# Kernel tuning notes

Hardware: AMD Instinct MI355X
Metric: run time of the kernel (lower is better)

The kernel has to match this reference:

```python
import jax, jax.numpy as jnp
import numpy as np

B, S, D = 2, 2048, 1024
H = 16
HD = D // H  # 64
ROPE_BASE = 10000.0


def rotate_half(x):
    x1, x2 = jnp.split(x, 2, axis=-1)
    return jnp.concatenate((-x2, x1), axis=-1)


def rope_cos_sin(seq_len, dim, dtype):
    inv_freq = 1.0 / (ROPE_BASE ** (jnp.arange(0, dim, 2, dtype=jnp.float32) / dim))
    t = jnp.arange(seq_len, dtype=jnp.float32)
    freqs = jnp.einsum('i,j->ij', t, inv_freq)          # [S, dim/2]
    emb = jnp.concatenate((freqs, freqs), axis=-1)      # [S, dim]
    return jnp.cos(emb).astype(dtype), jnp.sin(emb).astype(dtype)


def setup_inputs() -> dict:
    key = jax.random.key(0)
    ks = jax.random.split(key, 5)
    std = 0.02
    return {
        'x': jax.random.normal(ks[0], (B, S, D), dtype=jnp.float32),
        'wq': jax.random.normal(ks[1], (D, D), dtype=jnp.float32) * std,
        'wk': jax.random.normal(ks[2], (D, D), dtype=jnp.float32) * std,
        'wv': jax.random.normal(ks[3], (D, D), dtype=jnp.float32) * std,
        'wo': jax.random.normal(ks[4], (D, D), dtype=jnp.float32) * std,
    }


def reference(x, wq, wk, wv, wo):
    b, s, d = x.shape
    # Q/K/V projections (nn.Linear: x @ W.T)
    q = jnp.einsum('bsd,ed->bse', x, wq).reshape(b, s, H, HD).transpose(0, 2, 1, 3)
    k = jnp.einsum('bsd,ed->bse', x, wk).reshape(b, s, H, HD).transpose(0, 2, 1, 3)
    v = jnp.einsum('bsd,ed->bse', x, wv).reshape(b, s, H, HD).transpose(0, 2, 1, 3)
    # RoPE
    cos, sin = rope_cos_sin(s, HD, x.dtype)  # [s, HD]
    cos = cos[None, None]  # [1,1,s,HD]
    sin = sin[None, None]
    q = q * cos + rotate_half(q) * sin
    k = k * cos + rotate_half(k) * sin
    # Causal SDPA
    scale = HD ** -0.5
    scores = jnp.einsum('bhqd,bhkd->bhqk', q, k) * scale
    causal = jnp.tril(jnp.ones((s, s), dtype=bool))
    scores = jnp.where(causal[None, None], scores, jnp.finfo(scores.dtype).min)
    attn = jax.nn.softmax(scores, axis=-1)
    out = jnp.einsum('bhqk,bhkd->bhqd', attn, v)
    out = out.transpose(0, 2, 1, 3).reshape(b, s, d)
    return jnp.einsum('bsd,ed->bse', out, wo)
```

## Files before the change

### kernel.cpp

```cpp
#include <hip/hip_runtime.h>
#include <hip/hip_bf16.h>
#include <cstdint>
#include <cstddef>

#define BDIM 2
#define SDIM 2048
#define DDIM 1024
#define HN   16
#define HDIM 64

using bf16 = __bf16;
typedef __attribute__((ext_vector_type(8))) __bf16 bf16x8;
typedef __attribute__((ext_vector_type(4))) __bf16 bf16x4;
typedef __attribute__((ext_vector_type(8))) unsigned short ushort8;
typedef __attribute__((ext_vector_type(4))) float  f32x4;

#define MFMA16(a, b, c) __builtin_amdgcn_mfma_f32_16x16x32_bf16((a), (b), (c), 0, 0, 0)

#define ASYNC16(g, l)                                                          \
  __builtin_amdgcn_global_load_lds(                                            \
      (const __attribute__((address_space(1))) void*)(g),                      \
      (__attribute__((address_space(3))) void*)(l), 16, 0, 0)

#define QSCALE 0.1803368801111204f

__global__ __launch_bounds__(256) void cvt_bf16(const float* __restrict__ src,
                                                bf16* __restrict__ dst, int n4) {
  int i = blockIdx.x * 256 + threadIdx.x;
  if (i < n4) {
    float4 v = ((const float4*)src)[i];
    bf16x4 o = {(__bf16)v.x, (__bf16)v.y, (__bf16)v.z, (__bf16)v.w};
    *(bf16x4*)(dst + (size_t)i * 4) = o;
  }
}

struct Ptr4 { const float* p[4]; };
__global__ __launch_bounds__(256) void cvt_w(Ptr4 srcs, bf16* __restrict__ dst) {
  const int seg = blockIdx.y;
  const float* src = srcs.p[seg];
  int i = blockIdx.x * 256 + threadIdx.x;
  float4 v = ((const float4*)src)[i];
  bf16x4 o = {(__bf16)v.x, (__bf16)v.y, (__bf16)v.z, (__bf16)v.w};
  *(bf16x4*)(dst + (size_t)seg * (DDIM * DDIM) + (size_t)i * 4) = o;
}

__global__ __launch_bounds__(256) void rope_table(float* __restrict__ cosT,
                                                  float* __restrict__ sinT) {
  int i = blockIdx.x * 256 + threadIdx.x;
  int s = i >> 5, j = i & 31;
  float inv = powf(10000.f, -(float)j * (1.f / 32.f));
  float a = (float)s * inv;
  float sn, c;
  sincosf(a, &sn, &c);
  cosT[s * 64 + j]      = c;
  cosT[s * 64 + j + 32] = c;
  sinT[s * 64 + j]      = sn;
  sinT[s * 64 + j + 32] = sn;
}

__global__ __launch_bounds__(256) void rope_apply(bf16* __restrict__ q,
                                                  bf16* __restrict__ k,
                                                  const float* __restrict__ cosT,
                                                  const float* __restrict__ sinT) {
  int i = blockIdx.x * 256 + threadIdx.x;
  int j = i & 31;
  int s = (i >> 5) & (SDIM - 1);
  int bh = i >> 16;
  size_t base = ((size_t)bh * SDIM + s) * HDIM;
  float c = cosT[s * 64 + j], sn = sinT[s * 64 + j];
  float a = (float)q[base + j], b2 = (float)q[base + j + 32];
  q[base + j]      = (__bf16)((a * c - b2 * sn) * QSCALE);
  q[base + j + 32] = (__bf16)((b2 * c + a * sn) * QSCALE);
  a = (float)k[base + j]; b2 = (float)k[base + j + 32];
  k[base + j]      = (__bf16)(a * c - b2 * sn);
  k[base + j + 32] = (__bf16)(b2 * c + a * sn);
}

__global__ __launch_bounds__(256) void transpose_v(const unsigned short* __restrict__ v,
                                                   unsigned short* __restrict__ vt) {
  const int bh = blockIdx.y;
  const int s_base = blockIdx.x * 32 + (threadIdx.x >> 6) * 8;
  const int d = threadIdx.x & 63;
  const unsigned short* src = v + ((size_t)bh * SDIM + s_base) * HDIM + d;
  ushort8 o;
#pragma unroll
  for (int j = 0; j < 8; ++j) o[j] = src[(size_t)j * HDIM];
  *(ushort8*)(vt + ((size_t)bh * HDIM + d) * SDIM + s_base) = o;
}

template <int MODE>
__global__ __launch_bounds__(256) void gemm_bt(const bf16* __restrict__ A,
                                               const bf16* __restrict__ B0,
                                               void* __restrict__ C0) {
  constexpr int K = 1024;
  __shared__ __align__(16) bf16 As[128 * 64];
  __shared__ __align__(16) bf16 Bs[128 * 64];
  const int tid = threadIdx.x;
  const int l = tid & 63, w = tid >> 6;
  const int wr = w >> 1, wc = w & 1;
  const int lr = l & 15, lg = l >> 4;
  const int bm = blockIdx.y * 128;
  const int bn = blockIdx.x * 128;
  const bf16* Bw = B0 + (size_t)blockIdx.z * (1024 * 1024);

  f32x4 acc[4][4] = {};

  for (int k0 = 0; k0 < K; k0 += 64) {
    __syncthreads();
#pragma unroll
    for (int i = 0; i < 4; ++i) {
      int idx = i * 2048 + tid * 8;
      int row = idx >> 6, col = idx & 63;
      ASYNC16(A + (size_t)(bm + row) * K + (k0 + col), As + idx);
      ASYNC16(Bw + (size_t)(bn + row) * K + (k0 + col), Bs + idx);
    }
    __syncthreads();
#pragma unroll
    for (int c = 0; c < 2; ++c) {
      bf16x8 af[4], bfr[4];
#pragma unroll
      for (int m = 0; m < 4; ++m)
        af[m] = *(const bf16x8*)(As + (wr * 64 + m * 16 + lr) * 64 + c * 32 + lg * 8);
#pragma unroll
      for (int n = 0; n < 4; ++n)
        bfr[n] = *(const bf16x8*)(Bs + (wc * 64 + n * 16 + lr) * 64 + c * 32 + lg * 8);
      __builtin_amdgcn_s_setprio(1);
#pragma unroll
      for (int m = 0; m < 4; ++m)
#pragma unroll
        for (int n = 0; n < 4; ++n)
          acc[m][n] = MFMA16(af[m], bfr[n], acc[m][n]);
      __builtin_amdgcn_s_setprio(0);
    }
  }

#pragma unroll
  for (int m = 0; m < 4; ++m) {
#pragma unroll
    for (int n = 0; n < 4; ++n) {
#pragma unroll
      for (int r = 0; r < 4; ++r) {
        int row = bm + wr * 64 + m * 16 + lg * 4 + r;
        int col = bn + wc * 64 + n * 16 + lr;
        float v = acc[m][n][r];
        if constexpr (MODE == 0) {
          bf16* C = (bf16*)C0 + (size_t)blockIdx.z * ((size_t)BDIM * SDIM * DDIM);
          size_t off = (((size_t)(row >> 11) * HN + (col >> 6)) * SDIM + (row & (SDIM - 1))) * HDIM + (col & 63);
          C[off] = (__bf16)v;
        } else {
          ((float*)C0)[(size_t)row * DDIM + col] = v;
        }
      }
    }
  }
}

__global__ __launch_bounds__(256) void attn_fwd(const bf16* __restrict__ qg,
                                                const bf16* __restrict__ kg,
                                                const bf16* __restrict__ vtg,
                                                bf16* __restrict__ og) {
  __shared__ __align__(16) bf16 Ks[2][8 * 512];
  __shared__ __align__(16) bf16 Vs[2][8 * 512];
  __shared__ __align__(16) bf16 Pl[4][16 * 72];

  const int tid = threadIdx.x;
  const int l = tid & 63, w = tid >> 6;
  const int lr = l & 15, lg = l >> 4;
  const int lin = blockIdx.x + (blockIdx.y << 4);
  const int bh = lin & 31;
  const int qp = lin >> 5;
  const size_t hb = (size_t)bh * SDIM * HDIM;
  const bf16* Q  = qg + hb;
  const bf16* Kp = kg + hb;
  const bf16* Vp = vtg + hb;
  const int b = bh >> 4, h = bh & 15;
  bf16* Pw = &Pl[w][0];

  const int mm0 = 2 * w, mm1 = 2 * w + 1;
  const int f0 = mm0 & 3, c0 = mm0 >> 2;
  const int f1 = mm1 & 3, c1 = mm1 >> 2;
  bf16* const kd0_0 = Ks[0] + mm0 * 512 + l * 8;
  bf16* const kd1_0 = Ks[0] + mm1 * 512 + l * 8;
  bf16* const vd0_0 = Vs[0] + mm0 * 512 + l * 8;
  bf16* const vd1_0 = Vs[0] + mm1 * 512 + l * 8;

  for (int phase = 0; phase < 2; ++phase) {
    const int qt = phase ? (31 - qp) : qp;
    const int q0 = qt * 64;

    bf16x8 qf[2];
#pragma unroll
    for (int c = 0; c < 2; ++c)
      qf[c] = *(const bf16x8*)(Q + (size_t)(q0 + w * 16 + lr) * HDIM + c * 32 + lg * 8);

    f32x4 o[4] = {};
    float m = -3e38f, lsum = 0.f;

    const bf16* kN0 = Kp + (size_t)(f0 * 16 + lr) * HDIM + c0 * 32 + lg * 8;
    const bf16* kN1 = Kp + (size_t)(f1 * 16 + lr) * HDIM + c1 * 32 + lg * 8;
    const bf16* vN0 = Vp + (size_t)(f0 * 16 + lr) * SDIM + c0 * 32 + lg * 8;
    const bf16* vN1 = Vp + (size_t)(f1 * 16 + lr) * SDIM + c1 * 32 + lg * 8;

    ASYNC16(kN0, kd0_0); kN0 += 64 * HDIM;
    ASYNC16(kN1, kd1_0); kN1 += 64 * HDIM;
    ASYNC16(vN0, vd0_0); vN0 += 64;
    ASYNC16(vN1, vd1_0); vN1 += 64;
    __syncthreads();

    for (int t = 0; t <= qt; ++t) {
      const int cur = t & 1;
      if (t < qt) {
        bf16* kd = Ks[cur ^ 1];
        bf16* vd = Vs[cur ^ 1];
        ASYNC16(kN0, kd + mm0 * 512 + l * 8); kN0 += 64 * HDIM;
        ASYNC16(kN1, kd + mm1 * 512 + l * 8); kN1 += 64 * HDIM;
        ASYNC16(vN0, vd + mm0 * 512 + l * 8); vN0 += 64;
        ASYNC16(vN1, vd + mm1 * 512 + l * 8); vN1 += 64;
      }

      const bool diag = (t == qt);
      const int fLim = diag ? w : 3;

      f32x4 sc[4] = {};
      __builtin_amdgcn_s_setprio(1);
#pragma unroll
      for (int c = 0; c < 2; ++c)
#pragma unroll
        for (int f = 0; f < 4; ++f)
          if (f <= fLim) {
            bf16x8 kfr = *(const bf16x8*)(Ks[cur] + (c * 4 + f) * 512 + l * 8);
            sc[f] = MFMA16(kfr, qf[c], sc[f]);
          }
      __builtin_amdgcn_s_setprio(0);

      if (diag) {
#pragma unroll
        for (int f = 0; f < 4; ++f)
#pragma unroll
          for (int r = 0; r < 4; ++r) {
            if (f > w)
              sc[f][r] = -3e38f;
            else if (f == w)
              sc[f][r] = (lg * 4 + r <= lr) ? sc[f][r] : -3e38f;
          }
      }

      float mx = -3e38f;
#pragma unroll
      for (int f = 0; f < 4; ++f)
#pragma unroll
        for (int r = 0; r < 4; ++r) mx = fmaxf(mx, sc[f][r]);
      mx = fmaxf(mx, __shfl_xor(mx, 16));
      mx = fmaxf(mx, __shfl_xor(mx, 32));

      if (!__all(mx - m <= 8.f)) {
        float mnew = fmaxf(m, mx);
        float corr = exp2f(m - mnew);
        m = mnew;
        lsum *= corr;
        float cb[4];
#pragma unroll
        for (int r = 0; r < 4; ++r) cb[r] = __shfl(corr, lg * 4 + r);
#pragma unroll
        for (int n = 0; n < 4; ++n)
#pragma unroll
          for (int r = 0; r < 4; ++r) o[n][r] *= cb[r];
      }

      float rs = 0.f;
#pragma unroll
      for (int f = 0; f < 4; ++f) {
        float p0 = exp2f(sc[f][0] - m);
        float p1 = exp2f(sc[f][1] - m);
        float p2 = exp2f(sc[f][2] - m);
        float p3 = exp2f(sc[f][3] - m);
        rs += (p0 + p1) + (p2 + p3);
        bf16x4 pv = {(__bf16)p0, (__bf16)p1, (__bf16)p2, (__bf16)p3};
        *(bf16x4*)(Pw + lr * 72 + f * 16 + lg * 4) = pv;
      }
      rs += __shfl_xor(rs, 16);
      rs += __shfl_xor(rs, 32);
      lsum += rs;

      const int cLim = diag ? (w >> 1) : 1;
      __builtin_amdgcn_s_setprio(1);
#pragma unroll
      for (int c = 0; c < 2; ++c)
        if (c <= cLim) {
          bf16x8 pf = *(const bf16x8*)(Pw + lr * 72 + c * 32 + lg * 8);
#pragma unroll
          for (int n = 0; n < 4; ++n) {
            bf16x8 vfr = *(const bf16x8*)(Vs[cur] + (c * 4 + n) * 512 + l * 8);
            o[n] = MFMA16(pf, vfr, o[n]);
          }
        }
      __builtin_amdgcn_s_setprio(0);

      __syncthreads();
    }

    float lb[4];
#pragma unroll
    for (int r = 0; r < 4; ++r) lb[r] = __shfl(lsum, lg * 4 + r);
#pragma unroll
    for (int r = 0; r < 4; ++r) {
      float rl = 1.f / lb[r];
      int qr = q0 + 16 * w + lg * 4 + r;
#pragma unroll
      for (int n = 0; n < 4; ++n)
        og[((size_t)(b * SDIM + qr)) * DDIM + h * HDIM + n * 16 + lr] =
            (__bf16)(o[n][r] * rl);
    }
  }
}

extern "C" void kernel_launch(void* const* d_in, const int* in_sizes, int n_in,
                              void* d_out, int out_size, void* d_ws, size_t ws_size,
                              hipStream_t stream) {
  const float* x  = (const float*)d_in[0];
  const float* wq = (const float*)d_in[1];
  const float* wk = (const float*)d_in[2];
  const float* wv = (const float*)d_in[3];
  const float* wo = (const float*)d_in[4];

  char* ws = (char*)d_ws;
  const size_t MB = 1024 * 1024;
  bf16* xb   = (bf16*)(ws + 0);
  bf16* wqb  = (bf16*)(ws + 8 * MB);
  bf16* wob  = (bf16*)(ws + 14 * MB);
  bf16* qb   = (bf16*)(ws + 16 * MB);
  bf16* kb   = (bf16*)(ws + 24 * MB);
  bf16* vb   = (bf16*)(ws + 32 * MB);
  bf16* ob   = (bf16*)(ws + 40 * MB);
  float* cosT = (float*)(ws + 48 * MB);
  float* sinT = (float*)(ws + 49 * MB);
  bf16* vtb  = xb;

  const int NX = BDIM * SDIM * DDIM;
  const int NW = DDIM * DDIM;

  cvt_bf16<<<NX / 4 / 256, 256, 0, stream>>>(x, xb, NX / 4);
  Ptr4 wsrc{{wq, wk, wv, wo}};
  cvt_w<<<dim3(NW / 4 / 256, 4), 256, 0, stream>>>(wsrc, wqb);
  rope_table<<<(SDIM * 32) / 256, 256, 0, stream>>>(cosT, sinT);
  gemm_bt<0><<<dim3(8, 32, 3), 256, 0, stream>>>(xb, wqb, (void*)qb);
  rope_apply<<<(32 * SDIM * 32) / 256, 256, 0, stream>>>(qb, kb, cosT, sinT);
  transpose_v<<<dim3(SDIM / 32, 32), 256, 0, stream>>>((const unsigned short*)vb,
                                                       (unsigned short*)vtb);
  attn_fwd<<<dim3(16, 32), 256, 0, stream>>>(qb, kb, vtb, ob);
  gemm_bt<1><<<dim3(8, 32, 1), 256, 0, stream>>>(ob, wob, d_out);
}
```

Before: 148.9 us.

## Fuse RoPE and V transpose into QKV GEMM epilogue

Applies RoPE (with the Q scale folded into a precomputed cos/sin table) directly in the QKV projection epilogue, pairing accumulator columns j and j+32 that the same wave holds. V is written already transposed from the GEMM epilogue, which removes the rope_apply and transpose_v kernels and their global memory round trips. The attention kernel also defers the cross-lane max shuffles until a rescale is actually needed. The epilogue stores become scattered, and the deferred max relies on a per-lane bound check staying conservative.

New measurement: 153.7 us. +3.2%, slower.

```diff
diff --git a/kernel.cpp b/kernel.cpp
--- a/kernel.cpp
+++ b/kernel.cpp
@@ -12,7 +12,6 @@
 using bf16 = __bf16;
 typedef __attribute__((ext_vector_type(8))) __bf16 bf16x8;
 typedef __attribute__((ext_vector_type(4))) __bf16 bf16x4;
-typedef __attribute__((ext_vector_type(8))) unsigned short ushort8;
 typedef __attribute__((ext_vector_type(4))) float  f32x4;
 
 #define MFMA16(a, b, c) __builtin_amdgcn_mfma_f32_16x16x32_bf16((a), (b), (c), 0, 0, 0)
@@ -44,54 +43,24 @@
   *(bf16x4*)(dst + (size_t)seg * (DDIM * DDIM) + (size_t)i * 4) = o;
 }
 
-__global__ __launch_bounds__(256) void rope_table(float* __restrict__ cosT,
-                                                  float* __restrict__ sinT) {
+__global__ __launch_bounds__(256) void rope_table(float2* __restrict__ cq,
+                                                  float2* __restrict__ ck) {
   int i = blockIdx.x * 256 + threadIdx.x;
   int s = i >> 5, j = i & 31;
   float inv = powf(10000.f, -(float)j * (1.f / 32.f));
   float a = (float)s * inv;
   float sn, c;
   sincosf(a, &sn, &c);
-  cosT[s * 64 + j]      = c;
-  cosT[s * 64 + j + 32] = c;
-  sinT[s * 64 + j]      = sn;
-  sinT[s * 64 + j + 32] = sn;
-}
-
-__global__ __launch_bounds__(256) void rope_apply(bf16* __restrict__ q,
-                                                  bf16* __restrict__ k,
-                                                  const float* __restrict__ cosT,
-                                                  const float* __restrict__ sinT) {
-  int i = blockIdx.x * 256 + threadIdx.x;
-  int j = i & 31;
-  int s = (i >> 5) & (SDIM - 1);
-  int bh = i >> 16;
-  size_t base = ((size_t)bh * SDIM + s) * HDIM;
-  float c = cosT[s * 64 + j], sn = sinT[s * 64 + j];
-  float a = (float)q[base + j], b2 = (float)q[base + j + 32];
-  q[base + j]      = (__bf16)((a * c - b2 * sn) * QSCALE);
-  q[base + j + 32] = (__bf16)((b2 * c + a * sn) * QSCALE);
-  a = (float)k[base + j]; b2 = (float)k[base + j + 32];
-  k[base + j]      = (__bf16)(a * c - b2 * sn);
-  k[base + j + 32] = (__bf16)(b2 * c + a * sn);
-}
-
-__global__ __launch_bounds__(256) void transpose_v(const unsigned short* __restrict__ v,
-                                                   unsigned short* __restrict__ vt) {
-  const int bh = blockIdx.y;
-  const int s_base = blockIdx.x * 32 + (threadIdx.x >> 6) * 8;
-  const int d = threadIdx.x & 63;
-  const unsigned short* src = v + ((size_t)bh * SDIM + s_base) * HDIM + d;
-  ushort8 o;
-#pragma unroll
-  for (int j = 0; j < 8; ++j) o[j] = src[(size_t)j * HDIM];
-  *(ushort8*)(vt + ((size_t)bh * HDIM + d) * SDIM + s_base) = o;
+  ck[i] = make_float2(c, sn);
+  cq[i] = make_float2(c * QSCALE, sn * QSCALE);
 }
 
 template <int MODE>
 __global__ __launch_bounds__(256) void gemm_bt(const bf16* __restrict__ A,
                                                const bf16* __restrict__ B0,
-                                               void* __restrict__ C0) {
+                                               void* __restrict__ C0,
+                                               const float2* __restrict__ cq,
+                                               const float2* __restrict__ ck) {
   constexpr int K = 1024;
   __shared__ __align__(16) bf16 As[128 * 64];
   __shared__ __align__(16) bf16 Bs[128 * 64];
@@ -134,24 +103,53 @@
     }
   }
 
-#pragma unroll
-  for (int m = 0; m < 4; ++m) {
-#pragma unroll
-    for (int n = 0; n < 4; ++n) {
-#pragma unroll
-      for (int r = 0; r < 4; ++r) {
-        int row = bm + wr * 64 + m * 16 + lg * 4 + r;
-        int col = bn + wc * 64 + n * 16 + lr;
-        float v = acc[m][n][r];
-        if constexpr (MODE == 0) {
-          bf16* C = (bf16*)C0 + (size_t)blockIdx.z * ((size_t)BDIM * SDIM * DDIM);
-          size_t off = (((size_t)(row >> 11) * HN + (col >> 6)) * SDIM + (row & (SDIM - 1))) * HDIM + (col & 63);
-          C[off] = (__bf16)v;
-        } else {
-          ((float*)C0)[(size_t)row * DDIM + col] = v;
+  if constexpr (MODE == 0) {
+    const int z = blockIdx.z;
+    bf16* C = (bf16*)C0 + (size_t)z * ((size_t)BDIM * SDIM * DDIM);
+    if (z == 2) {
+#pragma unroll
+      for (int m = 0; m < 4; ++m)
+#pragma unroll
+        for (int n = 0; n < 4; ++n) {
+          int row0 = bm + wr * 64 + m * 16 + lg * 4;
+          int col  = bn + wc * 64 + n * 16 + lr;
+          int bb = row0 >> 11, s0 = row0 & (SDIM - 1);
+          int h = col >> 6, hd = col & 63;
+          bf16x4 pv = {(__bf16)acc[m][n][0], (__bf16)acc[m][n][1],
+                       (__bf16)acc[m][n][2], (__bf16)acc[m][n][3]};
+          *(bf16x4*)(C + ((size_t)(bb * HN + h) * HDIM + hd) * SDIM + s0) = pv;
         }
-      }
-    }
+    } else {
+      const float2* tab = z ? ck : cq;
+#pragma unroll
+      for (int m = 0; m < 4; ++m)
+#pragma unroll
+        for (int n = 0; n < 2; ++n) {
+          int j = n * 16 + lr;
+          int h = (bn >> 6) + wc;
+#pragma unroll
+          for (int r = 0; r < 4; ++r) {
+            int row = bm + wr * 64 + m * 16 + lg * 4 + r;
+            int s = row & (SDIM - 1), bb = row >> 11;
+            float2 cs = tab[s * 32 + j];
+            float a = acc[m][n][r], b2 = acc[m][n + 2][r];
+            size_t base = ((size_t)(bb * HN + h) * SDIM + s) * HDIM;
+            C[base + j]      = (__bf16)(a * cs.x - b2 * cs.y);
+            C[base + j + 32] = (__bf16)(b2 * cs.x + a * cs.y);
+          }
+        }
+    }
+  } else {
+#pragma unroll
+    for (int m = 0; m < 4; ++m)
+#pragma unroll
+      for (int n = 0; n < 4; ++n)
+#pragma unroll
+        for (int r = 0; r < 4; ++r) {
+          int row = bm + wr * 64 + m * 16 + lg * 4 + r;
+          int col = bn + wc * 64 + n * 16 + lr;
+          ((float*)C0)[(size_t)row * DDIM + col] = acc[m][n][r];
+        }
   }
 }
 
@@ -245,15 +243,15 @@
           }
       }
 
-      float mx = -3e38f;
+      float mxl = -3e38f;
 #pragma unroll
       for (int f = 0; f < 4; ++f)
 #pragma unroll
-        for (int r = 0; r < 4; ++r) mx = fmaxf(mx, sc[f][r]);
-      mx = fmaxf(mx, __shfl_xor(mx, 16));
-      mx = fmaxf(mx, __shfl_xor(mx, 32));
-
-      if (!__all(mx - m <= 8.f)) {
+        for (int r = 0; r < 4; ++r) mxl = fmaxf(mxl, sc[f][r]);
+
+      if (!__all(mxl - m <= 8.f)) {
+        float mx = fmaxf(mxl, __shfl_xor(mxl, 16));
+        mx = fmaxf(mx, __shfl_xor(mx, 32));
         float mnew = fmaxf(m, mx);
         float corr = exp2f(m - mnew);
         m = mnew;
@@ -330,11 +328,10 @@
   bf16* wob  = (bf16*)(ws + 14 * MB);
   bf16* qb   = (bf16*)(ws + 16 * MB);
   bf16* kb   = (bf16*)(ws + 24 * MB);
-  bf16* vb   = (bf16*)(ws + 32 * MB);
+  bf16* vtb  = (bf16*)(ws + 32 * MB);
   bf16* ob   = (bf16*)(ws + 40 * MB);
-  float* cosT = (float*)(ws + 48 * MB);
-  float* sinT = (float*)(ws + 49 * MB);
-  bf16* vtb  = xb;
+  float2* cqT = (float2*)(ws + 48 * MB);
+  float2* ckT = (float2*)(ws + 48 * MB + 512 * 1024);
 
   const int NX = BDIM * SDIM * DDIM;
   const int NW = DDIM * DDIM;
@@ -342,11 +339,8 @@
   cvt_bf16<<<NX / 4 / 256, 256, 0, stream>>>(x, xb, NX / 4);
   Ptr4 wsrc{{wq, wk, wv, wo}};
   cvt_w<<<dim3(NW / 4 / 256, 4), 256, 0, stream>>>(wsrc, wqb);
-  rope_table<<<(SDIM * 32) / 256, 256, 0, stream>>>(cosT, sinT);
-  gemm_bt<0><<<dim3(8, 32, 3), 256, 0, stream>>>(xb, wqb, (void*)qb);
-  rope_apply<<<(32 * SDIM * 32) / 256, 256, 0, stream>>>(qb, kb, cosT, sinT);
-  transpose_v<<<dim3(SDIM / 32, 32), 256, 0, stream>>>((const unsigned short*)vb,
-                                                       (unsigned short*)vtb);
+  rope_table<<<(SDIM * 32) / 256, 256, 0, stream>>>(cqT, ckT);
+  gemm_bt<0><<<dim3(8, 32, 3), 256, 0, stream>>>(xb, wqb, (void*)qb, cqT, ckT);
   attn_fwd<<<dim3(16, 32), 256, 0, stream>>>(qb, kb, vtb, ob);
-  gemm_bt<1><<<dim3(8, 32, 1), 256, 0, stream>>>(ob, wob, d_out);
-}
+  gemm_bt<1><<<dim3(8, 32, 1), 256, 0, stream>>>(ob, wob, d_out, nullptr, nullptr);
+}
```

## Launch one block per query tile with longest-first order and swizzled P buffer

Applied to the files above, without the earlier changes.

Each attention block used to process two paired query tiles (qp and 31-qp) to balance the causal work. Now every block handles a single query tile, so the grid doubles to 1024 blocks, ordered so the heaviest (largest qt) tiles go out first. The P scratch buffer drops its 72-element padding in favour of an XOR swizzle to avoid LDS bank conflicts. The max reduction across lanes is also moved inside the rescale branch, so the common path skips two shuffles. The trade-off is losing the explicit pairing balance and relying on the hardware scheduler to even out tile lengths.

Measured after the change: 145.8 us. 2.1% less time.

```diff
diff --git a/kernel.cpp b/kernel.cpp
--- a/kernel.cpp
+++ b/kernel.cpp
@@ -161,156 +161,149 @@
                                                 bf16* __restrict__ og) {
   __shared__ __align__(16) bf16 Ks[2][8 * 512];
   __shared__ __align__(16) bf16 Vs[2][8 * 512];
-  __shared__ __align__(16) bf16 Pl[4][16 * 72];
+  __shared__ __align__(16) bf16 Pl[4][16 * 64];
 
   const int tid = threadIdx.x;
   const int l = tid & 63, w = tid >> 6;
   const int lr = l & 15, lg = l >> 4;
-  const int lin = blockIdx.x + (blockIdx.y << 4);
-  const int bh = lin & 31;
-  const int qp = lin >> 5;
+  const int bh = blockIdx.x;
+  const int qt = 31 - blockIdx.y;
+  const int q0 = qt * 64;
   const size_t hb = (size_t)bh * SDIM * HDIM;
   const bf16* Q  = qg + hb;
   const bf16* Kp = kg + hb;
   const bf16* Vp = vtg + hb;
   const int b = bh >> 4, h = bh & 15;
   bf16* Pw = &Pl[w][0];
+  const int swz = lr & 7;
 
   const int mm0 = 2 * w, mm1 = 2 * w + 1;
   const int f0 = mm0 & 3, c0 = mm0 >> 2;
   const int f1 = mm1 & 3, c1 = mm1 >> 2;
-  bf16* const kd0_0 = Ks[0] + mm0 * 512 + l * 8;
-  bf16* const kd1_0 = Ks[0] + mm1 * 512 + l * 8;
-  bf16* const vd0_0 = Vs[0] + mm0 * 512 + l * 8;
-  bf16* const vd1_0 = Vs[0] + mm1 * 512 + l * 8;
-
-  for (int phase = 0; phase < 2; ++phase) {
-    const int qt = phase ? (31 - qp) : qp;
-    const int q0 = qt * 64;
-
-    bf16x8 qf[2];
+
+  bf16x8 qf[2];
+#pragma unroll
+  for (int c = 0; c < 2; ++c)
+    qf[c] = *(const bf16x8*)(Q + (size_t)(q0 + w * 16 + lr) * HDIM + c * 32 + lg * 8);
+
+  f32x4 o[4] = {};
+  float m = -3e38f, lsum = 0.f;
+
+  const bf16* kN0 = Kp + (size_t)(f0 * 16 + lr) * HDIM + c0 * 32 + lg * 8;
+  const bf16* kN1 = Kp + (size_t)(f1 * 16 + lr) * HDIM + c1 * 32 + lg * 8;
+  const bf16* vN0 = Vp + (size_t)(f0 * 16 + lr) * SDIM + c0 * 32 + lg * 8;
+  const bf16* vN1 = Vp + (size_t)(f1 * 16 + lr) * SDIM + c1 * 32 + lg * 8;
+
+  ASYNC16(kN0, Ks[0] + mm0 * 512 + l * 8); kN0 += 64 * HDIM;
+  ASYNC16(kN1, Ks[0] + mm1 * 512 + l * 8); kN1 += 64 * HDIM;
+  ASYNC16(vN0, Vs[0] + mm0 * 512 + l * 8); vN0 += 64;
+  ASYNC16(vN1, Vs[0] + mm1 * 512 + l * 8); vN1 += 64;
+  __syncthreads();
+
+  for (int t = 0; t <= qt; ++t) {
+    const int cur = t & 1;
+    if (t < qt) {
+      bf16* kd = Ks[cur ^ 1];
+      bf16* vd = Vs[cur ^ 1];
+      ASYNC16(kN0, kd + mm0 * 512 + l * 8); kN0 += 64 * HDIM;
+      ASYNC16(kN1, kd + mm1 * 512 + l * 8); kN1 += 64 * HDIM;
+      ASYNC16(vN0, vd + mm0 * 512 + l * 8); vN0 += 64;
+      ASYNC16(vN1, vd + mm1 * 512 + l * 8); vN1 += 64;
+    }
+
+    const bool diag = (t == qt);
+    const int fLim = diag ? w : 3;
+
+    f32x4 sc[4] = {};
+    __builtin_amdgcn_s_setprio(1);
 #pragma unroll
     for (int c = 0; c < 2; ++c)
-      qf[c] = *(const bf16x8*)(Q + (size_t)(q0 + w * 16 + lr) * HDIM + c * 32 + lg * 8);
-
-    f32x4 o[4] = {};
-    float m = -3e38f, lsum = 0.f;
-
-    const bf16* kN0 = Kp + (size_t)(f0 * 16 + lr) * HDIM + c0 * 32 + lg * 8;
-    const bf16* kN1 = Kp + (size_t)(f1 * 16 + lr) * HDIM + c1 * 32 + lg * 8;
-    const bf16* vN0 = Vp + (size_t)(f0 * 16 + lr) * SDIM + c0 * 32 + lg * 8;
-    const bf16* vN1 = Vp + (size_t)(f1 * 16 + lr) * SDIM + c1 * 32 + lg * 8;
-
-    ASYNC16(kN0, kd0_0); kN0 += 64 * HDIM;
-    ASYNC16(kN1, kd1_0); kN1 += 64 * HDIM;
-    ASYNC16(vN0, vd0_0); vN0 += 64;
-    ASYNC16(vN1, vd1_0); vN1 += 64;
+#pragma unroll
+      for (int f = 0; f < 4; ++f)
+        if (f <= fLim) {
+          bf16x8 kfr = *(const bf16x8*)(Ks[cur] + (c * 4 + f) * 512 + l * 8);
+          sc[f] = MFMA16(kfr, qf[c], sc[f]);
+        }
+    __builtin_amdgcn_s_setprio(0);
+
+    if (diag) {
+#pragma unroll
+      for (int f = 0; f < 4; ++f)
+#pragma unroll
+        for (int r = 0; r < 4; ++r) {
+          if (f > w)
+            sc[f][r] = -3e38f;
+          else if (f == w)
+            sc[f][r] = (lg * 4 + r <= lr) ? sc[f][r] : -3e38f;
+        }
+    }
+
+    float mxl = -3e38f;
+#pragma unroll
+    for (int f = 0; f < 4; ++f)
+#pragma unroll
+      for (int r = 0; r < 4; ++r) mxl = fmaxf(mxl, sc[f][r]);
+
+    if (!__all(mxl - m <= 8.f)) {
+      float mx = fmaxf(mxl, __shfl_xor(mxl, 16));
+      mx = fmaxf(mx, __shfl_xor(mx, 32));
+      float mnew = fmaxf(m, mx);
+      float corr = exp2f(m - mnew);
+      m = mnew;
+      lsum *= corr;
+      float cb[4];
+#pragma unroll
+      for (int r = 0; r < 4; ++r) cb[r] = __shfl(corr, lg * 4 + r);
+#pragma unroll
+      for (int n = 0; n < 4; ++n)
+#pragma unroll
+        for (int r = 0; r < 4; ++r) o[n][r] *= cb[r];
+    }
+
+    float rs = 0.f;
+#pragma unroll
+    for (int f = 0; f < 4; ++f) {
+      float p0 = exp2f(sc[f][0] - m);
+      float p1 = exp2f(sc[f][1] - m);
+      float p2 = exp2f(sc[f][2] - m);
+      float p3 = exp2f(sc[f][3] - m);
+      rs += (p0 + p1) + (p2 + p3);
+      bf16x4 pv = {(__bf16)p0, (__bf16)p1, (__bf16)p2, (__bf16)p3};
+      const int ch = f * 2 + (lg >> 1);
+      *(bf16x4*)(Pw + lr * 64 + ((ch ^ swz) << 3) + (lg & 1) * 4) = pv;
+    }
+    rs += __shfl_xor(rs, 16);
+    rs += __shfl_xor(rs, 32);
+    lsum += rs;
+
+    const int cLim = diag ? (w >> 1) : 1;
+    __builtin_amdgcn_s_setprio(1);
+#pragma unroll
+    for (int c = 0; c < 2; ++c)
+      if (c <= cLim) {
+        bf16x8 pf = *(const bf16x8*)(Pw + lr * 64 + (((c * 4 + lg) ^ swz) << 3));
+#pragma unroll
+        for (int n = 0; n < 4; ++n) {
+          bf16x8 vfr = *(const bf16x8*)(Vs[cur] + (c * 4 + n) * 512 + l * 8);
+          o[n] = MFMA16(pf, vfr, o[n]);
+        }
+      }
+    __builtin_amdgcn_s_setprio(0);
+
     __syncthreads();
-
-    for (int t = 0; t <= qt; ++t) {
-      const int cur = t & 1;
-      if (t < qt) {
-        bf16* kd = Ks[cur ^ 1];
-        bf16* vd = Vs[cur ^ 1];
-        ASYNC16(kN0, kd + mm0 * 512 + l * 8); kN0 += 64 * HDIM;
-        ASYNC16(kN1, kd + mm1 * 512 + l * 8); kN1 += 64 * HDIM;
-        ASYNC16(vN0, vd + mm0 * 512 + l * 8); vN0 += 64;
-        ASYNC16(vN1, vd + mm1 * 512 + l * 8); vN1 += 64;
-      }
-
-      const bool diag = (t == qt);
-      const int fLim = diag ? w : 3;
-
-      f32x4 sc[4] = {};
-      __builtin_amdgcn_s_setprio(1);
-#pragma unroll
-      for (int c = 0; c < 2; ++c)
-#pragma unroll
-        for (int f = 0; f < 4; ++f)
-          if (f <= fLim) {
-            bf16x8 kfr = *(const bf16x8*)(Ks[cur] + (c * 4 + f) * 512 + l * 8);
-            sc[f] = MFMA16(kfr, qf[c], sc[f]);
-          }
-      __builtin_amdgcn_s_setprio(0);
-
-      if (diag) {
-#pragma unroll
-        for (int f = 0; f < 4; ++f)
-#pragma unroll
-          for (int r = 0; r < 4; ++r) {
-            if (f > w)
-              sc[f][r] = -3e38f;
-            else if (f == w)
-              sc[f][r] = (lg * 4 + r <= lr) ? sc[f][r] : -3e38f;
-          }
-      }
-
-      float mx = -3e38f;
-#pragma unroll
-      for (int f = 0; f < 4; ++f)
-#pragma unroll
-        for (int r = 0; r < 4; ++r) mx = fmaxf(mx, sc[f][r]);
-      mx = fmaxf(mx, __shfl_xor(mx, 16));
-      mx = fmaxf(mx, __shfl_xor(mx, 32));
-
-      if (!__all(mx - m <= 8.f)) {
-        float mnew = fmaxf(m, mx);
-        float corr = exp2f(m - mnew);
-        m = mnew;
-        lsum *= corr;
-        float cb[4];
-#pragma unroll
-        for (int r = 0; r < 4; ++r) cb[r] = __shfl(corr, lg * 4 + r);
-#pragma unroll
-        for (int n = 0; n < 4; ++n)
-#pragma unroll
-          for (int r = 0; r < 4; ++r) o[n][r] *= cb[r];
-      }
-
-      float rs = 0.f;
-#pragma unroll
-      for (int f = 0; f < 4; ++f) {
-        float p0 = exp2f(sc[f][0] - m);
-        float p1 = exp2f(sc[f][1] - m);
-        float p2 = exp2f(sc[f][2] - m);
-        float p3 = exp2f(sc[f][3] - m);
-        rs += (p0 + p1) + (p2 + p3);
-        bf16x4 pv = {(__bf16)p0, (__bf16)p1, (__bf16)p2, (__bf16)p3};
-        *(bf16x4*)(Pw + lr * 72 + f * 16 + lg * 4) = pv;
-      }
-      rs += __shfl_xor(rs, 16);
-      rs += __shfl_xor(rs, 32);
-      lsum += rs;
-
-      const int cLim = diag ? (w >> 1) : 1;
-      __builtin_amdgcn_s_setprio(1);
-#pragma unroll
-      for (int c = 0; c < 2; ++c)
-        if (c <= cLim) {
-          bf16x8 pf = *(const bf16x8*)(Pw + lr * 72 + c * 32 + lg * 8);
-#pragma unroll
-          for (int n = 0; n < 4; ++n) {
-            bf16x8 vfr = *(const bf16x8*)(Vs[cur] + (c * 4 + n) * 512 + l * 8);
-            o[n] = MFMA16(pf, vfr, o[n]);
-          }
-        }
-      __builtin_amdgcn_s_setprio(0);
-
-      __syncthreads();
-    }
-
-    float lb[4];
-#pragma unroll
-    for (int r = 0; r < 4; ++r) lb[r] = __shfl(lsum, lg * 4 + r);
-#pragma unroll
-    for (int r = 0; r < 4; ++r) {
-      float rl = 1.f / lb[r];
-      int qr = q0 + 16 * w + lg * 4 + r;
-#pragma unroll
-      for (int n = 0; n < 4; ++n)
-        og[((size_t)(b * SDIM + qr)) * DDIM + h * HDIM + n * 16 + lr] =
-            (__bf16)(o[n][r] * rl);
-    }
+  }
+
+  float lb[4];
+#pragma unroll
+  for (int r = 0; r < 4; ++r) lb[r] = __shfl(lsum, lg * 4 + r);
+#pragma unroll
+  for (int r = 0; r < 4; ++r) {
+    float rl = 1.f / lb[r];
+    int qr = q0 + 16 * w + lg * 4 + r;
+#pragma unroll
+    for (int n = 0; n < 4; ++n)
+      og[((size_t)(b * SDIM + qr)) * DDIM + h * HDIM + n * 16 + lr] =
+          (__bf16)(o[n][r] * rl);
   }
 }
 
@@ -347,6 +340,6 @@
   rope_apply<<<(32 * SDIM * 32) / 256, 256, 0, stream>>>(qb, kb, cosT, sinT);
   transpose_v<<<dim3(SDIM / 32, 32), 256, 0, stream>>>((const unsigned short*)vb,
                                                        (unsigned short*)vtb);
-  attn_fwd<<<dim3(16, 32), 256, 0, stream>>>(qb, kb, vtb, ob);
+  attn_fwd<<<dim3(32, 32), 256, 0, stream>>>(qb, kb, vtb, ob);
   gemm_bt<1><<<dim3(8, 32, 1), 256, 0, stream>>>(ob, wob, d_out);
 }
```
